# Kernel tuning notes

Measured on AMD Instinct MI355X. Metric: run time of the kernel, lower is better.

## Reference

```python
import jax, jax.numpy as jnp
import numpy as np
import math

HIDDEN = 2048
HEADS = 16
HEAD_DIM = HIDDEN // HEADS
SEQ = 2048
BATCH = 1
THRESH = 0.7


def setup_inputs() -> dict:
    key = jax.random.key(0)
    ks = jax.random.split(key, 9)
    init = lambda k, shape: (jax.random.normal(k, shape, dtype=jnp.float32) * 0.02)
    return {
        "hidden_states": jax.random.normal(ks[0], (BATCH, SEQ, HIDDEN), dtype=jnp.float32),
        "Wq": init(ks[1], (HIDDEN, HIDDEN)), "bq": jnp.zeros((HIDDEN,), jnp.float32),
        "Wk": init(ks[2], (HIDDEN, HIDDEN)), "bk": jnp.zeros((HIDDEN,), jnp.float32),
        "Wv": init(ks[3], (HIDDEN, HIDDEN)), "bv": jnp.zeros((HIDDEN,), jnp.float32),
        "Wo": init(ks[4], (HIDDEN, HIDDEN)), "bo": jnp.zeros((HIDDEN,), jnp.float32),
        "truth_gate": jnp.full((1,), THRESH, jnp.float32),
        "balance_gate": jnp.full((1,), THRESH, jnp.float32),
        "order_gate": jnp.full((1,), THRESH, jnp.float32),
        "justice_gate": jnp.full((1,), THRESH, jnp.float32),
        "harmony_gate": jnp.full((1,), THRESH, jnp.float32),
    }


def reference(hidden_states, Wq, bq, Wk, bk, Wv, bv, Wo, bo,
              truth_gate, balance_gate, order_gate, justice_gate, harmony_gate):
    B, S, D = hidden_states.shape
    H, hd = HEADS, HEAD_DIM
    # projections -> [B, H, S, hd]
    def proj(W, b):
        return (hidden_states @ W.T + b).reshape(B, S, H, hd).transpose(0, 2, 1, 3)
    q, k, v = proj(Wq, bq), proj(Wk, bk), proj(Wv, bv)

    scores = jnp.einsum('bhqd,bhkd->bhqk', q, k) / math.sqrt(hd)  # [B,H,S,S]

    # truth: penalize by key norm, broadcast over query axis? No -- k_norm is [B,H,S,1],
    # matching torch broadcasting: per-QUERY-row constant (k indexed like q rows).
    truth_penalty = jax.nn.sigmoid(truth_gate) * (jnp.linalg.norm(k, axis=-1, keepdims=True) * 0.01)

    # balance: row entropy of softmax(scores)
    logp = jax.nn.log_softmax(scores, axis=-1)
    entropy = -jnp.sum(jnp.exp(logp) * logp, axis=-1, keepdims=True)  # [B,H,S,1]
    balance_adjustment = jax.nn.sigmoid(balance_gate) * (entropy / math.log(S) * 0.1)

    # order: position bias over the LAST (key) axis, shape [1,1,S] in torch -> broadcasts on key dim
    position_bias = jnp.arange(S, dtype=jnp.float32) / S  # [S]
    order_bonus = jax.nn.sigmoid(order_gate) * (position_bias * 0.05)  # broadcasts over bhq,k

    # justice: pull scores toward their row mean
    mean_score = scores.mean(axis=-1, keepdims=True)
    justice_adjustment = jax.nn.sigmoid(justice_gate) * ((mean_score - scores) * 0.1)

    # harmony: negative mean abs diff along key axis, per row
    smoothness = -jnp.abs(scores[..., 1:] - scores[..., :-1]).mean(axis=-1, keepdims=True)
    harmony_smooth = jax.nn.sigmoid(harmony_gate) * (smoothness * 0.1)

    scores = scores - truth_penalty + balance_adjustment + order_bonus + justice_adjustment + harmony_smooth

    attn = jax.nn.softmax(scores, axis=-1)
    out = jnp.einsum('bhqk,bhkd->bhqd', attn, v)  # [B,H,S,hd]
    out = out.transpose(0, 2, 1, 3).reshape(B, S, D)
    return out @ Wo.T + bo
```

## Files before the change

### kernel.cpp

```cpp
#include <hip/hip_runtime.h>

typedef __bf16 bf16x8 __attribute__((ext_vector_type(8)));
typedef __bf16 bf16x4 __attribute__((ext_vector_type(4)));
typedef float f32x4 __attribute__((ext_vector_type(4)));

typedef const __attribute__((address_space(1))) void* gas_t;
typedef __attribute__((address_space(3))) void* las_t;

static constexpr int DIM = 2048;
static constexpr size_t MAT = (size_t)DIM * DIM;

__device__ __forceinline__ float sigmoidf_(float x) { return 1.f / (1.f + __expf(-x)); }

__global__ void cvt_kernel(const float* __restrict__ x, const float* __restrict__ wq,
                           const float* __restrict__ wk, const float* __restrict__ wv,
                           const float* __restrict__ wo, __bf16* __restrict__ dst) {
  const float* s;
  switch (blockIdx.y) {
    case 0: s = x; break;
    case 1: s = wq; break;
    case 2: s = wk; break;
    case 3: s = wv; break;
    default: s = wo; break;
  }
  __bf16* d = dst + (size_t)blockIdx.y * MAT;
  size_t i = ((size_t)blockIdx.x * 256 + threadIdx.x) * 4;
  float4 v = *(const float4*)(s + i);
  bf16x4 ov;
  ov[0] = (__bf16)v.x; ov[1] = (__bf16)v.y; ov[2] = (__bf16)v.z; ov[3] = (__bf16)v.w;
  *(bf16x4*)(d + i) = ov;
}

template <bool F32OUT, int BN>
__device__ __forceinline__ void gemm128(const __bf16* __restrict__ A, const __bf16* __restrict__ B,
                                        const float* __restrict__ bias, bool bias_row, float scale,
                                        void* __restrict__ Cout, int mtile, int ntile,
                                        __bf16* Asm, __bf16* Bsm) {
  constexpr int NJ = BN / 32;
  const int t = threadIdx.x, lane = t & 63, w = t >> 6;
  const int wrow = (w >> 1) * 64, wcol = (w & 1) * (BN / 2);
  const int rbase = mtile * 128, cbase = ntile * BN;
  f32x4 acc[4][NJ] = {};

  for (int k0 = 0; k0 < DIM; k0 += 32) {
    __syncthreads();
#pragma unroll
    for (int i = 0; i < 2; ++i) {
      const int o = i * 4096 + w * 1024 + lane * 16;
      const int r = o >> 6;
      const int ke = (o & 63) >> 1;
      __builtin_amdgcn_global_load_lds((gas_t)(A + (size_t)(rbase + r) * DIM + k0 + ke),
                                       (las_t)(Asm + (o >> 1)), 16, 0, 0);
    }
#pragma unroll
    for (int i = 0; i < BN / 64; ++i) {
      const int o = i * 4096 + w * 1024 + lane * 16;
      const int r = o >> 6;
      const int ke = (o & 63) >> 1;
      __builtin_amdgcn_global_load_lds((gas_t)(B + (size_t)(cbase + r) * DIM + k0 + ke),
                                       (las_t)(Bsm + (o >> 1)), 16, 0, 0);
    }
    __syncthreads();

    bf16x8 af[4], bf[NJ];
#pragma unroll
    for (int i = 0; i < 4; ++i)
      af[i] = *(const bf16x8*)(Asm + (wrow + i * 16 + (lane & 15)) * 32 + (lane >> 4) * 8);
#pragma unroll
    for (int j = 0; j < NJ; ++j)
      bf[j] = *(const bf16x8*)(Bsm + (wcol + j * 16 + (lane & 15)) * 32 + (lane >> 4) * 8);
#pragma unroll
    for (int i = 0; i < 4; ++i)
#pragma unroll
      for (int j = 0; j < NJ; ++j)
        acc[i][j] = __builtin_amdgcn_mfma_f32_16x16x32_bf16(af[i], bf[j], acc[i][j], 0, 0, 0);
  }

#pragma unroll
  for (int i = 0; i < 4; ++i)
#pragma unroll
    for (int j = 0; j < NJ; ++j)
#pragma unroll
      for (int r = 0; r < 4; ++r) {
        const int row = rbase + wrow + i * 16 + (lane >> 4) * 4 + r;
        const int col = cbase + wcol + j * 16 + (lane & 15);
        float v = acc[i][j][r] + (bias_row ? bias[row] : bias[col]);
        v *= scale;
        if (F32OUT)
          ((float*)Cout)[(size_t)row * DIM + col] = v;
        else
          ((__bf16*)Cout)[(size_t)row * DIM + col] = (__bf16)v;
      }
}

__global__ __launch_bounds__(256, 2) void qkv_kernel(
    const __bf16* __restrict__ Xb, const __bf16* __restrict__ Wqb, const __bf16* __restrict__ Wkb,
    const __bf16* __restrict__ Wvb, const float* __restrict__ bq, const float* __restrict__ bk,
    const float* __restrict__ bv, const float* __restrict__ jgate, __bf16* __restrict__ Qo,
    __bf16* __restrict__ Ko, __bf16* __restrict__ Vto) {
  __shared__ __bf16 Asm[128 * 32];
  __shared__ __bf16 Bsm[128 * 32];
  const int sel = blockIdx.x >> 4, nt = blockIdx.x & 15, mt = blockIdx.y;
  const __bf16 *A, *B;
  const float* bias;
  __bf16* C;
  bool brow = false;
  float sc = 1.f;
  if (sel == 0) {
    A = Xb; B = Wqb; bias = bq; C = Qo;
    sc = (1.f - 0.1f * sigmoidf_(jgate[0])) * 0.08838834764831843f;
  } else if (sel == 1) {
    A = Xb; B = Wkb; bias = bk; C = Ko;
  } else {
    A = Wvb; B = Xb; bias = bv; C = Vto; brow = true;
  }
  gemm128<false, 128>(A, B, bias, brow, sc, C, mt, nt, Asm, Bsm);
}

__global__ __launch_bounds__(256, 2) void outproj_kernel(const __bf16* __restrict__ Ab,
                                                         const __bf16* __restrict__ Wob,
                                                         const float* __restrict__ bo,
                                                         float* __restrict__ Cout) {
  __shared__ __bf16 Asm[128 * 32];
  __shared__ __bf16 Bsm[64 * 32];
  gemm128<true, 64>(Ab, Wob, bo, false, 1.f, Cout, blockIdx.y, blockIdx.x, Asm, Bsm);
}

__global__ __launch_bounds__(512) void attn_kernel(const __bf16* __restrict__ Q,
                                                   const __bf16* __restrict__ Kg,
                                                   const __bf16* __restrict__ VT,
                                                   const float* __restrict__ ogate,
                                                   __bf16* __restrict__ O) {
  __shared__ __bf16 Ks[2][4 * 64 * 32];
  __shared__ __bf16 Vs[2][2 * 128 * 32];
  __shared__ __bf16 Ps[8 * 16 * 64];
  const int t = threadIdx.x, lane = t & 63, w = t >> 6;
  const int h = blockIdx.y, qt = blockIdx.x;
  const float beta = sigmoidf_(ogate[0]) * 0.05f / 2048.0f;

  const int rs8 = (((lane >> 4) ^ ((lane >> 1) & 3)) & 3) * 8;

  const int qrow = qt * 128 + w * 16 + (lane & 15);
  bf16x8 qf[4];
#pragma unroll
  for (int c = 0; c < 4; ++c)
    qf[c] = *(const bf16x8*)(Q + (size_t)qrow * DIM + h * 128 + c * 32 + (lane >> 4) * 8);

  f32x4 oacc[8] = {};
  float m_r[4], l_r[4];
#pragma unroll
  for (int r = 0; r < 4; ++r) { m_r[r] = -1e30f; l_r[r] = 0.f; }

  auto stage = [&](int buf, int kt) {
#pragma unroll
    for (int i = 0; i < 2; ++i) {
      const int o = i * 8192 + w * 1024 + lane * 16;
      const int oz = o ^ (((o >> 7) & 3) << 4);
      const int ke = (oz & 63) >> 1;
      const int c = oz >> 12, key = (oz & 4095) >> 6;
      __builtin_amdgcn_global_load_lds(
          (gas_t)(Kg + (size_t)(kt + key) * DIM + h * 128 + c * 32 + ke),
          (las_t)(&Ks[buf][0] + (o >> 1)), 16, 0, 0);
      const int d = (o & 8191) >> 6;
      __builtin_amdgcn_global_load_lds(
          (gas_t)(VT + (size_t)(h * 128 + d) * DIM + kt + i * 32 + ke),
          (las_t)(&Vs[buf][0] + (o >> 1)), 16, 0, 0);
    }
  };

  stage(0, 0);
  int p = 0;
  for (int kt = 0; kt < 2048; kt += 64) {
    __syncthreads();
    if (kt + 64 < 2048) stage(p ^ 1, kt + 64);

    __builtin_amdgcn_s_setprio(1);
    f32x4 sc[4];
#pragma unroll
    for (int j = 0; j < 4; ++j) {
      f32x4 a = {};
#pragma unroll
      for (int c = 0; c < 4; ++c) {
        bf16x8 kf = *(const bf16x8*)(&Ks[p][0] + c * 2048 + (j * 16 + (lane & 15)) * 32 + rs8);
        a = __builtin_amdgcn_mfma_f32_16x16x32_bf16(qf[c], kf, a, 0, 0, 0);
      }
      sc[j] = a;
    }
    __builtin_amdgcn_s_setprio(0);
#pragma unroll
    for (int j = 0; j < 4; ++j) {
      const float pb = beta * (float)(kt + j * 16 + (lane & 15));
#pragma unroll
      for (int r = 0; r < 4; ++r) sc[j][r] += pb;
    }
    float rmax[4];
#pragma unroll
    for (int r = 0; r < 4; ++r)
      rmax[r] = fmaxf(fmaxf(sc[0][r], sc[1][r]), fmaxf(sc[2][r], sc[3][r]));
#pragma unroll
    for (int msk = 1; msk < 16; msk <<= 1)
#pragma unroll
      for (int r = 0; r < 4; ++r) rmax[r] = fmaxf(rmax[r], __shfl_xor(rmax[r], msk, 64));

    bool need = (rmax[0] > m_r[0]) | (rmax[1] > m_r[1]) |
                (rmax[2] > m_r[2]) | (rmax[3] > m_r[3]);
    if (__any(need)) {
#pragma unroll
      for (int r = 0; r < 4; ++r) {
        const float mn = fmaxf(m_r[r], rmax[r]);
        const float al = __expf(m_r[r] - mn);
        m_r[r] = mn;
        l_r[r] *= al;
#pragma unroll
        for (int d = 0; d < 8; ++d) oacc[d][r] *= al;
      }
    }
#pragma unroll
    for (int j = 0; j < 4; ++j)
#pragma unroll
      for (int r = 0; r < 4; ++r) sc[j][r] = __expf(sc[j][r] - m_r[r]);

    float rs[4];
#pragma unroll
    for (int r = 0; r < 4; ++r) rs[r] = (sc[0][r] + sc[1][r]) + (sc[2][r] + sc[3][r]);
#pragma unroll
    for (int msk = 1; msk < 16; msk <<= 1)
#pragma unroll
      for (int r = 0; r < 4; ++r) rs[r] += __shfl_xor(rs[r], msk, 64);
#pragma unroll
    for (int r = 0; r < 4; ++r) l_r[r] += rs[r];

    {
      __bf16* pw = Ps + w * 1024;
#pragma unroll
      for (int j = 0; j < 4; ++j)
#pragma unroll
        for (int r = 0; r < 4; ++r) {
          const int q = (lane >> 4) * 4 + r;
          pw[(q * 64 + j * 16 + (lane & 15)) ^ ((q & 7) << 3)] = (__bf16)sc[j][r];
        }
    }

    __builtin_amdgcn_s_setprio(1);
#pragma unroll
    for (int cc = 0; cc < 2; ++cc) {
      const int pe = (w * 1024 + (lane & 15) * 64 + cc * 32 + (lane >> 4) * 8) ^ ((lane & 7) << 3);
      bf16x8 pa = *(const bf16x8*)(Ps + pe);
#pragma unroll
      for (int d = 0; d < 8; ++d) {
        bf16x8 vf = *(const bf16x8*)(&Vs[p][0] + cc * 4096 + (d * 16 + (lane & 15)) * 32 + rs8);
        oacc[d] = __builtin_amdgcn_mfma_f32_16x16x32_bf16(pa, vf, oacc[d], 0, 0, 0);
      }
    }
    __builtin_amdgcn_s_setprio(0);
    p ^= 1;
  }

#pragma unroll
  for (int d = 0; d < 8; ++d)
#pragma unroll
    for (int r = 0; r < 4; ++r) {
      const int row = qt * 128 + w * 16 + (lane >> 4) * 4 + r;
      const int col = h * 128 + d * 16 + (lane & 15);
      O[(size_t)row * DIM + col] = (__bf16)(oacc[d][r] / l_r[r]);
    }
}

extern "C" void kernel_launch(void* const* d_in, const int* in_sizes, int n_in,
                              void* d_out, int out_size, void* d_ws, size_t ws_size,
                              hipStream_t stream) {
  const float* X  = (const float*)d_in[0];
  const float* Wq = (const float*)d_in[1];
  const float* bq = (const float*)d_in[2];
  const float* Wk = (const float*)d_in[3];
  const float* bk = (const float*)d_in[4];
  const float* Wv = (const float*)d_in[5];
  const float* bv = (const float*)d_in[6];
  const float* Wo = (const float*)d_in[7];
  const float* bo = (const float*)d_in[8];
  const float* order_g   = (const float*)d_in[11];
  const float* justice_g = (const float*)d_in[12];

  __bf16* wsb = (__bf16*)d_ws;
  __bf16* Xb  = wsb + 0 * MAT;
  __bf16* Wqb = wsb + 1 * MAT;
  __bf16* Wkb = wsb + 2 * MAT;
  __bf16* Wvb = wsb + 3 * MAT;
  __bf16* Wob = wsb + 4 * MAT;
  __bf16* Qb  = wsb + 5 * MAT;
  __bf16* Kb  = wsb + 6 * MAT;
  __bf16* VTb = wsb + 7 * MAT;
  __bf16* Ab  = Xb;

  cvt_kernel<<<dim3(4096, 5), 256, 0, stream>>>(X, Wq, Wk, Wv, Wo, wsb);
  qkv_kernel<<<dim3(48, 16), 256, 0, stream>>>(Xb, Wqb, Wkb, Wvb, bq, bk, bv, justice_g,
                                               Qb, Kb, VTb);
  attn_kernel<<<dim3(16, 16), 512, 0, stream>>>(Qb, Kb, VTb, order_g, Ab);
  outproj_kernel<<<dim3(32, 16), 256, 0, stream>>>(Ab, Wob, bo, (float*)d_out);
}
```

Baseline: 321.0 us.

## Deepen GEMM K-tile to 64 with XOR-swizzled LDS; simplify attention rescale

The shared GEMM helper now stages 64-wide K slices instead of 32, halving the number of barrier-separated iterations. It uses an XOR swizzle on the LDS layout to avoid bank conflicts on fragment reads, at the cost of doubling LDS per block. In the attention kernel, the setprio hints are removed. The conditional wave-vote online-softmax rescale is replaced by an unconditional rescale of l and the output accumulators, which removes a branch but adds multiplies every tile.

```diff
diff --git a/kernel.cpp b/kernel.cpp
--- a/kernel.cpp
+++ b/kernel.cpp
@@ -40,40 +40,45 @@
   const int t = threadIdx.x, lane = t & 63, w = t >> 6;
   const int wrow = (w >> 1) * 64, wcol = (w & 1) * (BN / 2);
   const int rbase = mtile * 128, cbase = ntile * BN;
+  const int rx8 = (lane & 7) << 3;
   f32x4 acc[4][NJ] = {};
 
-  for (int k0 = 0; k0 < DIM; k0 += 32) {
+  for (int k0 = 0; k0 < DIM; k0 += 64) {
     __syncthreads();
 #pragma unroll
-    for (int i = 0; i < 2; ++i) {
-      const int o = i * 4096 + w * 1024 + lane * 16;
-      const int r = o >> 6;
-      const int ke = (o & 63) >> 1;
+    for (int i = 0; i < 4; ++i) {
+      const int o = i * 4096 + t * 16;
+      const int r = o >> 7;
+      const int ke = ((o ^ ((r & 7) << 4)) & 127) >> 1;
       __builtin_amdgcn_global_load_lds((gas_t)(A + (size_t)(rbase + r) * DIM + k0 + ke),
                                        (las_t)(Asm + (o >> 1)), 16, 0, 0);
     }
 #pragma unroll
-    for (int i = 0; i < BN / 64; ++i) {
-      const int o = i * 4096 + w * 1024 + lane * 16;
-      const int r = o >> 6;
-      const int ke = (o & 63) >> 1;
+    for (int i = 0; i < BN / 32; ++i) {
+      const int o = i * 4096 + t * 16;
+      const int r = o >> 7;
+      const int ke = ((o ^ ((r & 7) << 4)) & 127) >> 1;
       __builtin_amdgcn_global_load_lds((gas_t)(B + (size_t)(cbase + r) * DIM + k0 + ke),
                                        (las_t)(Bsm + (o >> 1)), 16, 0, 0);
     }
     __syncthreads();
 
-    bf16x8 af[4], bf[NJ];
-#pragma unroll
-    for (int i = 0; i < 4; ++i)
-      af[i] = *(const bf16x8*)(Asm + (wrow + i * 16 + (lane & 15)) * 32 + (lane >> 4) * 8);
-#pragma unroll
-    for (int j = 0; j < NJ; ++j)
-      bf[j] = *(const bf16x8*)(Bsm + (wcol + j * 16 + (lane & 15)) * 32 + (lane >> 4) * 8);
-#pragma unroll
-    for (int i = 0; i < 4; ++i)
+#pragma unroll
+    for (int hh = 0; hh < 2; ++hh) {
+      const int kb = hh * 32 + (lane >> 4) * 8;
+      bf16x8 af[4], bf[NJ];
+#pragma unroll
+      for (int i = 0; i < 4; ++i)
+        af[i] = *(const bf16x8*)(Asm + (wrow + i * 16 + (lane & 15)) * 64 + (kb ^ rx8));
 #pragma unroll
       for (int j = 0; j < NJ; ++j)
-        acc[i][j] = __builtin_amdgcn_mfma_f32_16x16x32_bf16(af[i], bf[j], acc[i][j], 0, 0, 0);
+        bf[j] = *(const bf16x8*)(Bsm + (wcol + j * 16 + (lane & 15)) * 64 + (kb ^ rx8));
+#pragma unroll
+      for (int i = 0; i < 4; ++i)
+#pragma unroll
+        for (int j = 0; j < NJ; ++j)
+          acc[i][j] = __builtin_amdgcn_mfma_f32_16x16x32_bf16(af[i], bf[j], acc[i][j], 0, 0, 0);
+    }
   }
 
 #pragma unroll
@@ -98,8 +103,8 @@
     const __bf16* __restrict__ Wvb, const float* __restrict__ bq, const float* __restrict__ bk,
     const float* __restrict__ bv, const float* __restrict__ jgate, __bf16* __restrict__ Qo,
     __bf16* __restrict__ Ko, __bf16* __restrict__ Vto) {
-  __shared__ __bf16 Asm[128 * 32];
-  __shared__ __bf16 Bsm[128 * 32];
+  __shared__ __bf16 Asm[128 * 64];
+  __shared__ __bf16 Bsm[128 * 64];
   const int sel = blockIdx.x >> 4, nt = blockIdx.x & 15, mt = blockIdx.y;
   const __bf16 *A, *B;
   const float* bias;
@@ -121,8 +126,8 @@
                                                          const __bf16* __restrict__ Wob,
                                                          const float* __restrict__ bo,
                                                          float* __restrict__ Cout) {
-  __shared__ __bf16 Asm[128 * 32];
-  __shared__ __bf16 Bsm[64 * 32];
+  __shared__ __bf16 Asm[128 * 64];
+  __shared__ __bf16 Bsm[64 * 64];
   gemm128<true, 64>(Ab, Wob, bo, false, 1.f, Cout, blockIdx.y, blockIdx.x, Asm, Bsm);
 }
 
@@ -174,7 +179,6 @@
     __syncthreads();
     if (kt + 64 < 2048) stage(p ^ 1, kt + 64);
 
-    __builtin_amdgcn_s_setprio(1);
     f32x4 sc[4];
 #pragma unroll
     for (int j = 0; j < 4; ++j) {
@@ -186,7 +190,6 @@
       }
       sc[j] = a;
     }
-    __builtin_amdgcn_s_setprio(0);
 #pragma unroll
     for (int j = 0; j < 4; ++j) {
       const float pb = beta * (float)(kt + j * 16 + (lane & 15));
@@ -202,18 +205,12 @@
 #pragma unroll
       for (int r = 0; r < 4; ++r) rmax[r] = fmaxf(rmax[r], __shfl_xor(rmax[r], msk, 64));
 
-    bool need = (rmax[0] > m_r[0]) | (rmax[1] > m_r[1]) |
-                (rmax[2] > m_r[2]) | (rmax[3] > m_r[3]);
-    if (__any(need)) {
-#pragma unroll
-      for (int r = 0; r < 4; ++r) {
-        const float mn = fmaxf(m_r[r], rmax[r]);
-        const float al = __expf(m_r[r] - mn);
-        m_r[r] = mn;
-        l_r[r] *= al;
-#pragma unroll
-        for (int d = 0; d < 8; ++d) oacc[d][r] *= al;
-      }
+    float al[4];
+#pragma unroll
+    for (int r = 0; r < 4; ++r) {
+      const float mn = fmaxf(m_r[r], rmax[r]);
+      al[r] = __expf(m_r[r] - mn);
+      m_r[r] = mn;
     }
 #pragma unroll
     for (int j = 0; j < 4; ++j)
@@ -228,7 +225,11 @@
 #pragma unroll
       for (int r = 0; r < 4; ++r) rs[r] += __shfl_xor(rs[r], msk, 64);
 #pragma unroll
-    for (int r = 0; r < 4; ++r) l_r[r] += rs[r];
+    for (int r = 0; r < 4; ++r) l_r[r] = l_r[r] * al[r] + rs[r];
+#pragma unroll
+    for (int d = 0; d < 8; ++d)
+#pragma unroll
+      for (int r = 0; r < 4; ++r) oacc[d][r] *= al[r];
 
     {
       __bf16* pw = Ps + w * 1024;
@@ -241,7 +242,6 @@
         }
     }
 
-    __builtin_amdgcn_s_setprio(1);
 #pragma unroll
     for (int cc = 0; cc < 2; ++cc) {
       const int pe = (w * 1024 + (lane & 15) * 64 + cc * 32 + (lane >> 4) * 8) ^ ((lane & 7) << 3);
@@ -252,7 +252,6 @@
         oacc[d] = __builtin_amdgcn_mfma_f32_16x16x32_bf16(pa, vf, oacc[d], 0, 0, 0);
       }
     }
-    __builtin_amdgcn_s_setprio(0);
     p ^= 1;
   }
 
```

Result: no change. 320.7 us (-0.1%).
